# Kernel tuning notes

Measured on AMD Instinct MI355X. Metric: run time of the kernel, lower is better.

Reference implementation:

```python
import jax, jax.numpy as jnp
import numpy as np
import math

FACTOR = 5


def setup_inputs() -> dict:
    key = jax.random.key(0)
    kq, kk, kv, ki = jax.random.split(key, 4)
    B, L, H, D = 4, 2048, 8, 64
    sample_k = min(FACTOR * int(np.ceil(np.log(L))), L)  # 40
    queries = jax.random.normal(kq, (B, L, H, D), jnp.float32)
    keys = jax.random.normal(kk, (B, L, H, D), jnp.float32)
    values = jax.random.normal(kv, (B, L, H, D), jnp.float32)
    # torch.randint(L_K, (L_Q, sample_k)) in _prob_QK, passed explicitly for determinism
    index_sample = jax.random.randint(ki, (L, sample_k), 0, L, dtype=jnp.int32)
    attn_mask = jnp.zeros((1,), jnp.bool_)  # unused when mask_flag=False
    return {"queries": queries, "keys": keys, "values": values,
            "attn_mask": attn_mask, "index_sample": index_sample}


def reference(queries, keys, values, attn_mask, index_sample):
    # queries/keys/values: [B, L, H, D] -> [B, H, L, D]
    B, L_Q, H, D = queries.shape
    L_K = keys.shape[1]
    Q = jnp.swapaxes(queries, 1, 2)
    K = jnp.swapaxes(keys, 1, 2)
    V = jnp.swapaxes(values, 1, 2)

    n_top = min(FACTOR * int(math.ceil(math.log(L_Q))), L_Q)

    # --- _prob_QK ---
    # K_sample: gather sampled keys per query position -> [B, H, L_Q, sample_k, D]
    K_sample = K[:, :, index_sample, :]
    # Q_K_sample: [B, H, L_Q, sample_k]
    Q_K_sample = jnp.einsum('bhld,bhlsd->bhls', Q, K_sample)
    # sparsity measure M: max - mean(sum/L_K) -> [B, H, L_Q]
    M = Q_K_sample.max(axis=-1) - Q_K_sample.sum(axis=-1) / L_K
    _, M_top = jax.lax.top_k(M, n_top)  # [B, H, n_top]
    # Q_reduce: [B, H, n_top, D]
    Q_reduce = jnp.take_along_axis(Q, M_top[..., None], axis=2)
    # scores over ALL keys for the top queries: [B, H, n_top, L_K]
    scores_top = jnp.einsum('bhud,bhkd->bhuk', Q_reduce, K)

    scale = 1.0 / math.sqrt(D)
    scores_top = scores_top * scale

    # --- _get_initial_context (mask_flag=False): mean of V broadcast over L_Q ---
    context = jnp.broadcast_to(V.mean(axis=2, keepdims=True), (B, H, L_Q, D))

    # --- _update_context: softmax over keys, attend, scatter into context ---
    attn = jax.nn.softmax(scores_top, axis=-1)
    out_sel = jnp.einsum('bhuk,bhkd->bhud', attn, V)  # [B, H, n_top, D]
    bidx = jnp.arange(B)[:, None, None]
    hidx = jnp.arange(H)[None, :, None]
    context = context.at[bidx, hidx, M_top].set(out_sel)
    return context  # [B, H, L_Q, D]
```

## Files before the change

kernel.cpp:

```cpp
#include <hip/hip_runtime.h>
#include <hip/hip_bf16.h>

constexpr int B = 4, L = 2048, H = 8, D = 64, S = 40, TOP = 40;
constexpr int NMB = B * H * L / 4;

__global__ __launch_bounds__(256) void kA(const float* __restrict__ Q, const float* __restrict__ K,
                                          const float* __restrict__ V, const int* __restrict__ idx,
                                          float* __restrict__ M, float* __restrict__ Vpart) {
    __shared__ float4 red[256];
    const int t = threadIdx.x;
    if (blockIdx.x < NMB) {
        int r = blockIdx.x * 4 + (t >> 6);
        int lane = t & 63;
        int sq = lane >> 4, dq = lane & 15;
        int b = r >> 14, h = (r >> 11) & 7, l = r & (L - 1);
        const float4 q4 = *(const float4*)&Q[(((b * L + l) * H + h) << 6) + dq * 4];
        int myidx = (lane < S) ? idx[l * S + lane] : 0;
        int ki[10];
        #pragma unroll
        for (int i = 0; i < 10; ++i) ki[i] = __shfl(myidx, i * 4 + sq, 64);
        float4 kv[10];
        #pragma unroll
        for (int i = 0; i < 10; ++i)
            kv[i] = *(const float4*)&K[(((b * L + ki[i]) * H + h) << 6) + dq * 4];
        float maxv = -3.4e38f, sumv = 0.f;
        #pragma unroll
        for (int i = 0; i < 10; ++i) {
            float p = q4.x * kv[i].x + q4.y * kv[i].y + q4.z * kv[i].z + q4.w * kv[i].w;
            p += __shfl_xor(p, 1); p += __shfl_xor(p, 2);
            p += __shfl_xor(p, 4); p += __shfl_xor(p, 8);
            maxv = fmaxf(maxv, p); sumv += p;
        }
        maxv = fmaxf(maxv, __shfl_xor(maxv, 16));
        maxv = fmaxf(maxv, __shfl_xor(maxv, 32));
        sumv += __shfl_xor(sumv, 16);
        sumv += __shfl_xor(sumv, 32);
        if (lane == 0) M[r] = maxv - sumv * (1.0f / (float)L);
    } else {
        int blk = blockIdx.x - NMB;
        int bh = blk >> 4, chunk = blk & 15;
        int b = bh >> 3, h = bh & 7;
        int d4 = t & 15, rr = t >> 4;
        int l0 = chunk * 128;
        float4 acc = make_float4(0.f, 0.f, 0.f, 0.f);
        #pragma unroll
        for (int s = 0; s < 8; ++s) {
            int l = l0 + rr + s * 16;
            float4 v = *(const float4*)&V[(((b * L + l) * H + h) << 6) + d4 * 4];
            acc.x += v.x; acc.y += v.y; acc.z += v.z; acc.w += v.w;
        }
        red[t] = acc;
        __syncthreads();
        #pragma unroll
        for (int off = 8; off > 0; off >>= 1) {
            if (rr < off) {
                float4 o = red[t + off * 16];
                red[t].x += o.x; red[t].y += o.y; red[t].z += o.z; red[t].w += o.w;
            }
            __syncthreads();
        }
        if (rr == 0) *(float4*)&Vpart[(bh * 16 + chunk) * 64 + d4 * 4] = red[t];
    }
}

__global__ __launch_bounds__(256) void kB(const float* __restrict__ M, const float* __restrict__ Vpart,
                                          int* __restrict__ Mtop, float* __restrict__ mean) {
    const int t = threadIdx.x;
    if (blockIdx.x < 32) {
        const int bh = blockIdx.x;
        const int lane = t & 63, wid = t >> 6;
        float v[8];
        #pragma unroll
        for (int j = 0; j < 8; ++j) v[j] = M[bh * L + j * 256 + t];
        float bv = v[0]; int bj = 0;
        #pragma unroll
        for (int j = 1; j < 8; ++j) if (v[j] > bv) { bv = v[j]; bj = j; }
        __shared__ float swv[4];
        __shared__ int   swi[4];
        __shared__ int   winS;
        for (int it = 0; it < TOP; ++it) {
            float cv = bv; int ci = bj * 256 + t;
            #pragma unroll
            for (int m = 1; m < 64; m <<= 1) {
                float ov = __shfl_xor(cv, m); int oi = __shfl_xor(ci, m);
                if (ov > cv || (ov == cv && oi < ci)) { cv = ov; ci = oi; }
            }
            if (lane == 0) { swv[wid] = cv; swi[wid] = ci; }
            __syncthreads();
            if (t == 0) {
                float fv = swv[0]; int fi = swi[0];
                #pragma unroll
                for (int w = 1; w < 4; ++w)
                    if (swv[w] > fv || (swv[w] == fv && swi[w] < fi)) { fv = swv[w]; fi = swi[w]; }
                Mtop[bh * TOP + it] = fi;
                winS = fi;
            }
            __syncthreads();
            const int wl = winS;
            if ((wl & 255) == t) {
                if ((wl >> 8) == 0) v[0] = -3.4e38f;
                if ((wl >> 8) == 1) v[1] = -3.4e38f;
                if ((wl >> 8) == 2) v[2] = -3.4e38f;
                if ((wl >> 8) == 3) v[3] = -3.4e38f;
                if ((wl >> 8) == 4) v[4] = -3.4e38f;
                if ((wl >> 8) == 5) v[5] = -3.4e38f;
                if ((wl >> 8) == 6) v[6] = -3.4e38f;
                if ((wl >> 8) == 7) v[7] = -3.4e38f;
                bv = v[0]; bj = 0;
                #pragma unroll
                for (int j = 1; j < 8; ++j) if (v[j] > bv) { bv = v[j]; bj = j; }
            }
        }
    } else {
        int bh = (blockIdx.x - 32) * 4 + (t >> 6);
        int d = t & 63;
        float s = 0.f;
        #pragma unroll
        for (int c = 0; c < 16; ++c) s += Vpart[(bh * 16 + c) * 64 + d];
        mean[bh * 64 + d] = s * (1.0f / (float)L);
    }
}

template <int CC>
__global__ __launch_bounds__(256, 4) void kC(const float* __restrict__ Q, const float* __restrict__ K,
                                             const float* __restrict__ V, const int* __restrict__ Mtop,
                                             const float* __restrict__ mean, float* __restrict__ Npart,
                                             float* __restrict__ Zpart, float* __restrict__ out) {
    constexpr int NCC = L / CC;
    constexpr int KPT = CC / 32;
    constexpr int LDK = CC + (KPT == 4 ? 4 : 2);
    constexpr int LDP = LDK;
    constexpr int LDV = 68;
    constexpr int KVSZ = (CC * LDV > 64 * LDK) ? CC * LDV : 64 * LDK;
    __shared__ float KV[KVSZ];
    __shared__ float Qs[TOP * 64];
    __shared__ float Ps[TOP * LDP];
    const int t = threadIdx.x;
    const int nsel = B * H * NCC;
    if (blockIdx.x >= nsel) {
        const int N4 = B * H * L * D / 4;
        const float4* m4 = (const float4*)mean;
        float4* o4 = (float4*)out;
        for (int i = (blockIdx.x - nsel) * 256 + t; i < N4; i += 2048 * 256) {
            int bh = i >> 15, d4 = i & 15;
            o4[i] = m4[bh * 16 + d4];
        }
        return;
    }
    const int bh = blockIdx.x / NCC, kc = blockIdx.x % NCC;
    const int b = bh >> 3, h = bh & 7;
    const int k0 = kc * CC;
    for (int i = t; i < CC * 16; i += 256) {
        int kk = i >> 4, d4 = i & 15;
        float4 kv = *(const float4*)&K[(((b * L + k0 + kk) * H + h) << 6) + d4 * 4];
        KV[(d4 * 4 + 0) * LDK + kk] = kv.x;
        KV[(d4 * 4 + 1) * LDK + kk] = kv.y;
        KV[(d4 * 4 + 2) * LDK + kk] = kv.z;
        KV[(d4 * 4 + 3) * LDK + kk] = kv.w;
    }
    for (int i = t; i < TOP * 16; i += 256) {
        int u = i >> 4, d4 = i & 15;
        int lsel = Mtop[bh * TOP + u];
        *(float4*)&Qs[u * 64 + d4 * 4] =
            *(const float4*)&Q[(((b * L + lsel) * H + h) << 6) + d4 * 4];
    }
    __syncthreads();
    const int k2 = t & 31, ug = t >> 5;
    float acc[5][KPT];
    #pragma unroll
    for (int j = 0; j < 5; ++j)
        #pragma unroll
        for (int p = 0; p < KPT; ++p) acc[j][p] = 0.f;
    #pragma unroll 4
    for (int d4 = 0; d4 < 16; ++d4) {
        float kr[4][KPT];
        #pragma unroll
        for (int rr = 0; rr < 4; ++rr)
            #pragma unroll
            for (int p = 0; p < KPT; ++p)
                kr[rr][p] = KV[(d4 * 4 + rr) * LDK + k2 * KPT + p];
        #pragma unroll
        for (int j = 0; j < 5; ++j) {
            float4 q4 = *(const float4*)&Qs[(ug * 5 + j) * 64 + d4 * 4];
            #pragma unroll
            for (int p = 0; p < KPT; ++p)
                acc[j][p] += q4.x * kr[0][p] + q4.y * kr[1][p] + q4.z * kr[2][p] + q4.w * kr[3][p];
        }
    }
    #pragma unroll
    for (int j = 0; j < 5; ++j) {
        int u = ug * 5 + j;
        float z = 0.f;
        #pragma unroll
        for (int p = 0; p < KPT; ++p) {
            float e = __expf(acc[j][p] * 0.125f - 16.0f);
            Ps[u * LDP + k2 * KPT + p] = e;
            z += e;
        }
        z += __shfl_xor(z, 1); z += __shfl_xor(z, 2); z += __shfl_xor(z, 4);
        z += __shfl_xor(z, 8); z += __shfl_xor(z, 16);
        if (k2 == 0) Zpart[(bh * TOP + u) * NCC + kc] = z;
    }
    __syncthreads();
    for (int i = t; i < CC * 16; i += 256) {
        int kk = i >> 4, d4 = i & 15;
        *(float4*)&KV[kk * LDV + d4 * 4] =
            *(const float4*)&V[(((b * L + k0 + kk) * H + h) << 6) + d4 * 4];
    }
    __syncthreads();
    const int d4v = t & 15, ug2 = t >> 4;
    float4 o0 = make_float4(0,0,0,0), o1 = make_float4(0,0,0,0), o2 = make_float4(0,0,0,0);
    #pragma unroll 4
    for (int kk = 0; kk < CC; ++kk) {
        float4 vv = *(const float4*)&KV[kk * LDV + d4v * 4];
        float e0 = Ps[ug2 * LDP + kk];
        float e1 = Ps[(ug2 + 16) * LDP + kk];
        o0.x += e0 * vv.x; o0.y += e0 * vv.y; o0.z += e0 * vv.z; o0.w += e0 * vv.w;
        o1.x += e1 * vv.x; o1.y += e1 * vv.y; o1.z += e1 * vv.z; o1.w += e1 * vv.w;
        if (ug2 < 8) {
            float e2 = Ps[(ug2 + 32) * LDP + kk];
            o2.x += e2 * vv.x; o2.y += e2 * vv.y; o2.z += e2 * vv.z; o2.w += e2 * vv.w;
        }
    }
    *(float4*)&Npart[((bh * TOP + ug2) * NCC + kc) * 64 + d4v * 4] = o0;
    *(float4*)&Npart[((bh * TOP + ug2 + 16) * NCC + kc) * 64 + d4v * 4] = o1;
    if (ug2 < 8)
        *(float4*)&Npart[((bh * TOP + ug2 + 32) * NCC + kc) * 64 + d4v * 4] = o2;
}

template <int NCC>
__global__ __launch_bounds__(256) void kD(const int* __restrict__ Mtop, const float* __restrict__ Npart,
                                          const float* __restrict__ Zpart, float* __restrict__ out) {
    const int t = threadIdx.x;
    const int g = blockIdx.x * 4 + (t >> 6);
    const int d = t & 63;
    const int bh = g / TOP;
    const int lsel = Mtop[g];
    float z = 0.f;
    #pragma unroll
    for (int c = 0; c < NCC; ++c) z += Zpart[g * NCC + c];
    float n = 0.f;
    #pragma unroll
    for (int c = 0; c < NCC; ++c) n += Npart[(g * NCC + c) * 64 + d];
    out[((bh * L + lsel) << 6) + d] = n / z;
}

__global__ void fill_ctx(const float* __restrict__ mean, float4* __restrict__ out) {
    const int N4 = B * H * L * D / 4;
    for (int i = blockIdx.x * 256 + threadIdx.x; i < N4; i += gridDim.x * 256) {
        int bh = i >> 15, d4 = i & 15;
        out[i] = ((const float4*)mean)[bh * 16 + d4];
    }
}
__global__ void sel_attn(const float* __restrict__ Q, const float* __restrict__ K,
                         const float* __restrict__ V, const int* __restrict__ Mtop,
                         float* __restrict__ out) {
    __shared__ float qs[D];
    __shared__ float p[L];
    __shared__ float red[256];
    int blk = blockIdx.x;
    int bh = blk / TOP, u = blk - bh * TOP;
    int b = bh >> 3, h = bh & 7;
    int t = threadIdx.x;
    int lsel = Mtop[bh * TOP + u];
    if (t < 64) qs[t] = Q[(((b * L + lsel) * H + h) << 6) + t];
    __syncthreads();
    float lsum = 0.f;
    for (int kk = 0; kk < 8; ++kk) {
        int k = kk * 256 + t;
        const float4* krow = (const float4*)&K[((b * L + k) * H + h) << 6];
        const float4* q4 = (const float4*)qs;
        float acc = 0.f;
        #pragma unroll
        for (int j = 0; j < 16; ++j) {
            float4 kv = krow[j]; float4 qv = q4[j];
            acc += qv.x * kv.x + qv.y * kv.y + qv.z * kv.z + qv.w * kv.w;
        }
        float e = __expf(acc * 0.125f - 16.0f);
        p[k] = e;
        lsum += e;
    }
    red[t] = lsum; __syncthreads();
    for (int off = 128; off > 0; off >>= 1) {
        if (t < off) red[t] += red[t + off];
        __syncthreads();
    }
    float inv = 1.0f / red[0];
    __syncthreads();
    int d = t & 63, c = t >> 6;
    float acc = 0.f;
    for (int k = c * 512; k < (c + 1) * 512; ++k)
        acc += p[k] * V[(((b * L + k) * H + h) << 6) + d];
    red[t] = acc; __syncthreads();
    if (t < 128) red[t] += red[t + 128];
    __syncthreads();
    if (t < 64) out[((bh * L + lsel) << 6) + t] = (red[t] + red[t + 64]) * inv;
}

extern "C" void kernel_launch(void* const* d_in, const int* in_sizes, int n_in,
                              void* d_out, int out_size, void* d_ws, size_t ws_size,
                              hipStream_t stream) {
    const float* Q = (const float*)d_in[0];
    const float* K = (const float*)d_in[1];
    const float* V = (const float*)d_in[2];
    const int* idx = (const int*)d_in[4];
    float* out = (float*)d_out;

    char* ws = (char*)d_ws;
    const size_t NPB1 = (size_t)B * H * TOP * 32 * 64 * 4;
    const size_t NPB2 = (size_t)B * H * TOP * 16 * 64 * 4;
    auto layout = [&](size_t npb, size_t& persist) {
        size_t e = 163840 + npb;
        persist = (e > 262144 ? e : 262144);
        return persist + 5120 + 8192 + 131072 + 3072;
    };
    size_t p1, p2, p3;
    size_t need1 = layout(NPB1, p1);
    size_t need2 = layout(NPB2, p2);
    size_t need3 = layout(0, p3);
    int tier = (ws_size >= need1) ? 1 : (ws_size >= need2) ? 2 : (ws_size >= need3) ? 3 : 0;
    size_t persist = (tier == 1) ? p1 : (tier == 2) ? p2 : p3;

    float* M     = (float*)ws;
    float* Zpart = (float*)ws;
    float* Npart = (float*)(ws + 163840);
    int*   Mtop  = (int*)(ws + persist);
    float* mean  = (float*)(ws + persist + 5120);
    float* Vpart = (float*)(ws + persist + 5120 + 8192);

    kA<<<NMB + 512, 256, 0, stream>>>(Q, K, V, idx, M, Vpart);
    kB<<<40, 256, 0, stream>>>(M, Vpart, Mtop, mean);
    if (tier == 1) {
        kC<64><<<B * H * 32 + 2048, 256, 0, stream>>>(Q, K, V, Mtop, mean, Npart, Zpart, out);
        kD<32><<<320, 256, 0, stream>>>(Mtop, Npart, Zpart, out);
    } else if (tier == 2) {
        kC<128><<<B * H * 16 + 2048, 256, 0, stream>>>(Q, K, V, Mtop, mean, Npart, Zpart, out);
        kD<16><<<320, 256, 0, stream>>>(Mtop, Npart, Zpart, out);
    } else {
        fill_ctx<<<2048, 256, 0, stream>>>(mean, (float4*)out);
        sel_attn<<<B * H * TOP, 256, 0, stream>>>(Q, K, V, Mtop, out);
    }
}
```

Before: 112.0 us.

## Remap kA blocks by XCD for L2 locality and prefetch V tile in kC

In kA, block indices are remapped so that consecutive block IDs, which are dealt round-robin across the 8 XCDs, put all blocks of a given (b,h) group on the same XCD. The intent is better L2 reuse of the K rows gathered for that head. In kC, the V tile is loaded into registers before the QK compute phase and written to shared memory afterwards, so global latency overlaps the score computation. This costs extra registers (VPT float4 per thread), which may lower occupancy under launch_bounds(256,4).

```diff
diff --git a/kernel.cpp b/kernel.cpp
--- a/kernel.cpp
+++ b/kernel.cpp
@@ -10,10 +10,14 @@
     __shared__ float4 red[256];
     const int t = threadIdx.x;
     if (blockIdx.x < NMB) {
-        int r = blockIdx.x * 4 + (t >> 6);
+        int n = blockIdx.x;
+        int xcd = n & 7, slot = n >> 3;
+        int bh = xcd * 4 + (slot & 3);
+        int lb = slot >> 2;
         int lane = t & 63;
         int sq = lane >> 4, dq = lane & 15;
-        int b = r >> 14, h = (r >> 11) & 7, l = r & (L - 1);
+        int b = bh >> 3, h = bh & 7;
+        int l = lb * 4 + (t >> 6);
         const float4 q4 = *(const float4*)&Q[(((b * L + l) * H + h) << 6) + dq * 4];
         int myidx = (lane < S) ? idx[l * S + lane] : 0;
         int ki[10];
@@ -35,10 +39,12 @@
         maxv = fmaxf(maxv, __shfl_xor(maxv, 32));
         sumv += __shfl_xor(sumv, 16);
         sumv += __shfl_xor(sumv, 32);
-        if (lane == 0) M[r] = maxv - sumv * (1.0f / (float)L);
+        if (lane == 0) M[bh * L + l] = maxv - sumv * (1.0f / (float)L);
     } else {
-        int blk = blockIdx.x - NMB;
-        int bh = blk >> 4, chunk = blk & 15;
+        int m = blockIdx.x - NMB;
+        int xcd = m & 7, slot = m >> 3;
+        int bh = xcd * 4 + (slot & 3);
+        int chunk = slot >> 2;
         int b = bh >> 3, h = bh & 7;
         int d4 = t & 15, rr = t >> 4;
         int l0 = chunk * 128;
@@ -132,6 +138,7 @@
     constexpr int LDP = LDK;
     constexpr int LDV = 68;
     constexpr int KVSZ = (CC * LDV > 64 * LDK) ? CC * LDV : 64 * LDK;
+    constexpr int VPT = CC * 16 / 256;
     __shared__ float KV[KVSZ];
     __shared__ float Qs[TOP * 64];
     __shared__ float Ps[TOP * LDP];
@@ -164,6 +171,13 @@
         *(float4*)&Qs[u * 64 + d4 * 4] =
             *(const float4*)&Q[(((b * L + lsel) * H + h) << 6) + d4 * 4];
     }
+    float4 vpre[VPT];
+    #pragma unroll
+    for (int p = 0; p < VPT; ++p) {
+        int i = p * 256 + t;
+        int kk = i >> 4, d4 = i & 15;
+        vpre[p] = *(const float4*)&V[(((b * L + k0 + kk) * H + h) << 6) + d4 * 4];
+    }
     __syncthreads();
     const int k2 = t & 31, ug = t >> 5;
     float acc[5][KPT];
@@ -202,10 +216,11 @@
         if (k2 == 0) Zpart[(bh * TOP + u) * NCC + kc] = z;
     }
     __syncthreads();
-    for (int i = t; i < CC * 16; i += 256) {
+    #pragma unroll
+    for (int p = 0; p < VPT; ++p) {
+        int i = p * 256 + t;
         int kk = i >> 4, d4 = i & 15;
-        *(float4*)&KV[kk * LDV + d4 * 4] =
-            *(const float4*)&V[(((b * L + k0 + kk) * H + h) << 6) + d4 * 4];
+        *(float4*)&KV[kk * LDV + d4 * 4] = vpre[p];
     }
     __syncthreads();
     const int d4v = t & 15, ug2 = t >> 4;
```

After: 113.3 us. Within noise of the previous version (+1.2%).
